# Optimization experiments

Measured on AMD Instinct MI355X. Metric: run time of the kernel, lower is better.

Reference implementation:

```python
import jax, jax.numpy as jnp
import numpy as np

NSAMPLES = [64, 32, 16, 8, 4]
TEMPERATURE = 1.0


def square_distance(src, dst):
    # src [B,N,C], dst [B,M,C] -> [B,N,M]
    d = -2.0 * jnp.einsum('bnc,bmc->bnm', src, dst)
    d = d + jnp.sum(src ** 2, -1)[:, :, None]
    d = d + jnp.sum(dst ** 2, -1)[:, None, :]
    return d


def knn_point(nsample, xyz, new_xyz):
    # indices of nsample nearest points in xyz for each query in new_xyz
    sqrdists = square_distance(new_xyz, xyz)           # [B,S,N]
    _, idx = jax.lax.top_k(-sqrdists, nsample)         # smallest distances
    return idx                                         # [B,S,nsample]


def index_points(points, idx):
    # points [B,N,C], idx [B,S,K] -> [B,S,K,C]
    B, S, K = idx.shape
    flat = idx.reshape(B, S * K)
    out = jnp.take_along_axis(points, flat[..., None], axis=1)
    return out.reshape(B, S, K, points.shape[-1])


def boundary_loss(labels, coords, feats, num_classes):
    onehot = jax.nn.one_hot(labels, num_classes, dtype=jnp.float32)  # [B,N,C]
    loss = jnp.float32(0.0)
    for i, (coord, feat) in enumerate(zip(coords, feats)):
        if i == 0:
            probability_labels = onehot
        else:
            kneighbors = i * 4
            nb_idx = knn_point(kneighbors, coords[0], coord)          # [B,Ni,k]
            probability_labels = index_points(onehot, nb_idx).mean(-2)  # [B,Ni,C]
        nsample = NSAMPLES[i]
        neighbor_indexs = knn_point(nsample, coord, coord)            # [B,Ni,ns]
        neighbor_labels = index_points(probability_labels, neighbor_indexs)  # [B,Ni,ns,C]
        neighbor_feats = index_points(feat, neighbor_indexs)          # [B,Ni,ns,D]
        center_label = jnp.argmax(probability_labels, -1)[:, :, None]  # [B,Ni,1]
        neighbor_label = jnp.argmax(neighbor_labels, -1)               # [B,Ni,ns]
        mask = (center_label == neighbor_label)                        # [B,Ni,ns] bool
        cnt = jnp.sum(mask.astype(jnp.int32), -1)
        point_mask = (cnt > 0) & (cnt < nsample)                       # [B,Ni]
        any_pm = jnp.any(point_mask)
        pm = point_mask.astype(jnp.float32)[:, :, None]                # [B,Ni,1]
        # pairwise feature distances to the nsample neighbors
        diff = feat[:, :, None, :] - neighbor_feats                    # [B,Ni,ns,D]
        dist = jnp.sqrt(jnp.sum(diff ** 2, -1) + 1e-6)                 # [B,Ni,ns]
        dist = -dist
        dist = dist - jnp.max(dist, -1, keepdims=True)
        dist = dist / TEMPERATURE
        exp = jnp.exp(dist)
        pos = jnp.sum(exp * mask.astype(jnp.float32) * pm)
        neg = jnp.sum(exp * pm)
        pos = jnp.where(any_pm, pos, 1.0)
        neg = jnp.where(any_pm, neg, 1.0)
        term = -jnp.log(pos / (neg + 1e-6))
        loss = loss + jnp.where(any_pm, term, 0.0)
    return loss


def setup_inputs() -> dict:
    key = jax.random.key(0)
    ks = jax.random.split(key, 12)
    B, N = 2, 4096
    sizes = [N, N // 4, N // 16, N // 64, N // 256]
    inp = {}
    inp['labels'] = jax.random.randint(ks[0], (B, N), 0, 21)
    for i, s in enumerate(sizes):
        inp[f'coord{i}'] = jax.random.normal(ks[1 + i], (B, s, 3), dtype=jnp.float32)
        inp[f'feat{i}'] = jax.random.normal(ks[6 + i], (B, s, 32), dtype=jnp.float32)
    inp['num_classes'] = 21
    return inp


def reference(labels, coord0, coord1, coord2, coord3, coord4,
              feat0, feat1, feat2, feat3, feat4, num_classes):
    coords = [coord0, coord1, coord2, coord3, coord4]
    feats = [feat0, feat1, feat2, feat3, feat4]
    return boundary_loss(labels, coords, feats, num_classes)
```

## Files before the change

kernel.cpp:

```cpp
#include <hip/hip_runtime.h>
#include <math.h>

#define WAVE 64
#define NC 21

__device__ __forceinline__ unsigned f32_ord(float f) {
    unsigned u = __float_as_uint(f);
    return (u & 0x80000000u) ? ~u : (u | 0x80000000u);
}

__device__ __forceinline__ int wave_sum_i32(int v) {
#pragma unroll
    for (int off = 32; off >= 1; off >>= 1)
        v += __shfl_xor(v, off, WAVE);
    return v;
}

__device__ __forceinline__ unsigned wave_min_u32(unsigned v) {
#pragma unroll
    for (int off = 32; off >= 1; off >>= 1) {
        unsigned o = (unsigned)__shfl_xor((int)v, off, WAVE);
        v = (o < v) ? o : v;
    }
    return v;
}

__device__ __forceinline__ unsigned wave_max_u32(unsigned v) {
#pragma unroll
    for (int off = 32; off >= 1; off >>= 1) {
        unsigned o = (unsigned)__shfl_xor((int)v, off, WAVE);
        v = (o > v) ? o : v;
    }
    return v;
}

__device__ __forceinline__ unsigned long long wave_min_u64(unsigned long long v) {
#pragma unroll
    for (int off = 32; off >= 1; off >>= 1) {
        unsigned long long o = __shfl_xor(v, off, WAVE);
        v = (o < v) ? o : v;
    }
    return v;
}

__device__ __forceinline__ float wave_max_f32(float v) {
#pragma unroll
    for (int off = 32; off >= 1; off >>= 1)
        v = fmaxf(v, __shfl_xor(v, off, WAVE));
    return v;
}

__device__ __forceinline__ float wave_sum_f32(float v) {
#pragma unroll
    for (int off = 32; off >= 1; off >>= 1)
        v += __shfl_xor(v, off, WAVE);
    return v;
}

__device__ __forceinline__ unsigned long long bitonic_sort64(
    unsigned long long v, int lane)
{
#pragma unroll
    for (int k = 2; k <= 64; k <<= 1) {
#pragma unroll
        for (int j = k >> 1; j > 0; j >>= 1) {
            unsigned long long o = __shfl_xor(v, j, WAVE);
            bool take_min = (((lane & j) == 0) == ((lane & k) == 0));
            unsigned long long mn = (v < o) ? v : o;
            unsigned long long mx = (v < o) ? o : v;
            v = take_min ? mn : mx;
        }
    }
    return v;
}

struct SelShm {
    unsigned long long cbuf[64];
    unsigned long long mw[4];
    int sel[64];
    int swv[4][4];
    unsigned smin[4], smax[4];
    int scnt, bcnt;
};

template <int NI, int NS>
__device__ __forceinline__ void block_topNS(
    const float4* __restrict__ pts,
    float qx, float qy, float qz, float nq,
    SelShm& shm, int tid)
{
    constexpr int NPL = (NI + 255) / 256;
    constexpr bool FULL = (NPL * 256 == NI);
    constexpr int CAP = 48;
    const int lane = tid & 63;
    const int wid = tid >> 6;
    const unsigned long long lmask = (1ull << lane) - 1ull;

    unsigned ok[NPL];
#pragma unroll
    for (int j = 0; j < NPL; ++j) {
        int g = j * 256 + tid;
        unsigned o = 0xFFFFFFFFu;
        if (FULL || g < NI) {
            float4 p = pts[g];
            float dot = qx * p.x + qy * p.y + qz * p.z;
            o = f32_ord(-2.0f * dot + nq + p.w);
        }
        ok[j] = o;
    }

    unsigned mn = 0xFFFFFFFFu, mx = 0u;
#pragma unroll
    for (int j = 0; j < NPL; ++j) {
        mn = (ok[j] < mn) ? ok[j] : mn;
        unsigned v = (ok[j] == 0xFFFFFFFFu) ? 0u : ok[j];
        mx = (v > mx) ? v : mx;
    }
    mn = wave_min_u32(mn);
    mx = wave_max_u32(mx);
    if (lane == 0) { shm.smin[wid] = mn; shm.smax[wid] = mx; }
    if (tid == 0)  { shm.scnt = 0; shm.bcnt = 0; }
    __syncthreads();
#pragma unroll
    for (int w = 0; w < 4; ++w) {
        unsigned a = shm.smin[w], b = shm.smax[w];
        mn = (a < mn) ? a : mn;
        mx = (b > mx) ? b : mx;
    }

    unsigned lo = mn, hi = mx;
    int cLo = 0, cHi = NI;
    int it = 0;
    while (lo < hi && (cHi - cLo) > CAP) {
        unsigned piv = lo + ((hi - lo) >> 1);
        int c = 0;
#pragma unroll
        for (int j = 0; j < NPL; ++j) c += (ok[j] <= piv) ? 1 : 0;
        c = wave_sum_i32(c);
        if (lane == 0) shm.swv[it & 3][wid] = c;
        __syncthreads();
        int tot = shm.swv[it & 3][0] + shm.swv[it & 3][1]
                + shm.swv[it & 3][2] + shm.swv[it & 3][3];
        if (tot >= NS) { hi = piv; cHi = tot; }
        else           { lo = piv + 1; cLo = tot; }
        ++it;
    }

    const int clt = cLo;
    const int R = NS - cLo;

#pragma unroll
    for (int j = 0; j < NPL; ++j) {
        bool s = ok[j] < lo;
        unsigned long long mk = __ballot(s);
        int n = __popcll(mk);
        if (n) {
            int wb = 0;
            if (lane == 0) wb = atomicAdd(&shm.scnt, n);
            wb = __shfl(wb, 0, WAVE);
            if (s) shm.sel[wb + __popcll(mk & lmask)] = j * 256 + tid;
        }
    }
#pragma unroll
    for (int j = 0; j < NPL; ++j) {
        bool s = (ok[j] >= lo) && (ok[j] <= hi);
        unsigned long long mk = __ballot(s);
        int n = __popcll(mk);
        if (n) {
            int wb = 0;
            if (lane == 0) wb = atomicAdd(&shm.bcnt, n);
            wb = __shfl(wb, 0, WAVE);
            int slot = wb + __popcll(mk & lmask);
            if (s && slot < 64)
                shm.cbuf[slot] =
                    ((unsigned long long)ok[j] << 32) | (unsigned)(j * 256 + tid);
        }
    }
    __syncthreads();
    int Bcnt = shm.bcnt;

    if (Bcnt <= 64) {
        if (wid == 0) {
            unsigned long long p = (lane < Bcnt) ? shm.cbuf[lane] : ~0ull;
            p = bitonic_sort64(p, lane);
            if (lane < R) shm.sel[clt + lane] = (int)(unsigned)p;
        }
        __syncthreads();
    } else {
        unsigned consumed = 0u;
        for (int r = 0; r < R; ++r) {
            unsigned long long mv = ~0ull;
#pragma unroll
            for (int j = 0; j < NPL; ++j) {
                bool s = (ok[j] >= lo) && (ok[j] <= hi) && !((consumed >> j) & 1u);
                unsigned long long p =
                    ((unsigned long long)ok[j] << 32) | (unsigned)(j * 256 + tid);
                mv = (s && p < mv) ? p : mv;
            }
            mv = wave_min_u64(mv);
            if (lane == 0) shm.mw[wid] = mv;
            __syncthreads();
            unsigned long long m0 = shm.mw[0], m1 = shm.mw[1];
            unsigned long long m2 = shm.mw[2], m3 = shm.mw[3];
            unsigned long long ta = (m0 < m1) ? m0 : m1;
            unsigned long long tb = (m2 < m3) ? m2 : m3;
            unsigned long long t = (ta < tb) ? ta : tb;
#pragma unroll
            for (int j = 0; j < NPL; ++j) {
                unsigned long long p =
                    ((unsigned long long)ok[j] << 32) | (unsigned)(j * 256 + tid);
                if (p == t) consumed |= 1u << j;
            }
            if (tid == 0) shm.sel[clt + r] = (int)(unsigned)t;
            __syncthreads();
        }
    }
}

template <int NQ, int K>
__device__ __forceinline__ void knn_level(
    const float* __restrict__ qc, const float4* __restrict__ pk0,
    const int* __restrict__ rl, int* __restrict__ out,
    int q, SelShm& shm, int tid)
{
    int b = q / NQ, qi = q - b * NQ;
    const float* qp = qc + ((long)b * NQ + qi) * 3;
    float qx = qp[0], qy = qp[1], qz = qp[2];
    float nq = qx * qx + qy * qy + qz * qz;
    block_topNS<4096, K>(pk0 + (long)b * 4096, qx, qy, qz, nq, shm, tid);
    if ((tid >> 6) == 0) {
        int lane = tid & 63;
        int lb = (lane < K) ? rl[(long)b * 4096 + shm.sel[lane]] : -1;
        int cnt = 0;
#pragma unroll
        for (int k = 0; k < K; ++k) {
            int lk = __shfl(lb, k, WAVE);
            cnt += (lk == lane) ? 1 : 0;
        }
        int key = (lane < NC) ? ((cnt << 8) | (255 - lane)) : 0;
#pragma unroll
        for (int off = 32; off >= 1; off >>= 1) {
            int o = __shfl_xor(key, off, WAVE);
            key = (o > key) ? o : key;
        }
        if (lane == 0) out[(long)b * NQ + qi] = 255 - (key & 255);
    }
}

template <int NI, int NS>
__device__ __forceinline__ void boundary_epilogue(
    const float* __restrict__ feat, const int* __restrict__ lbl,
    double* __restrict__ pos, double* __restrict__ neg, int* __restrict__ anyf,
    int b, int qi, int lane, int nb)
{
    int center = lbl[(long)b * NI + qi];
    bool m = false;
    float dj = -INFINITY;
    if (lane < NS) {
        m = (lbl[(long)b * NI + nb] == center);
        const float4* fq = (const float4*)(feat + ((long)b * NI + qi) * 32);
        const float4* fn = (const float4*)(feat + ((long)b * NI + nb) * 32);
        float s = 0.f;
#pragma unroll
        for (int d = 0; d < 8; ++d) {
            float4 a = fq[d], c = fn[d];
            float d0 = a.x - c.x, d1 = a.y - c.y;
            float d2 = a.z - c.z, d3 = a.w - c.w;
            s += d0 * d0 + d1 * d1 + d2 * d2 + d3 * d3;
        }
        dj = -sqrtf(s + 1e-6f);
    }
    unsigned long long mb = __ballot(m);
    int cnt = __popcll(mb);
    float mxv = wave_max_f32(dj);
    float ej = 0.f, pj = 0.f;
    if (lane < NS) {
        ej = expf(dj - mxv);
        pj = m ? ej : 0.f;
    }
    float se = wave_sum_f32(ej);
    float sp = wave_sum_f32(pj);
    bool pm = (cnt > 0) && (cnt < NS);
    if (pm && lane == 0) {
        atomicAdd(pos, (double)sp);
        atomicAdd(neg, (double)se);
        *anyf = 1;
    }
}

template <int NI, int NS>
__device__ __forceinline__ void boundary_level(
    const float4* __restrict__ pk, const float* __restrict__ coord,
    const float* __restrict__ feat, const int* __restrict__ lbl,
    double* __restrict__ pos, double* __restrict__ neg, int* __restrict__ anyf,
    int q, SelShm& shm, int tid)
{
    int b = q / NI, qi = q - b * NI;
    const float* qp = coord + ((long)b * NI + qi) * 3;
    float qx = qp[0], qy = qp[1], qz = qp[2];
    float nq = qx * qx + qy * qy + qz * qz;
    block_topNS<NI, NS>(pk + (long)b * NI, qx, qy, qz, nq, shm, tid);
    if ((tid >> 6) == 0)
        boundary_epilogue<NI, NS>(feat, lbl, pos, neg, anyf,
                                  b, qi, tid & 63, shm.sel[tid & 63]);
}

template <int NI, int NS>
__device__ __forceinline__ void small_boundary_level(
    const float4* __restrict__ pk, const float* __restrict__ coord,
    const float* __restrict__ feat, const int* __restrict__ lbl,
    double* __restrict__ pos, double* __restrict__ neg, int* __restrict__ anyf,
    int q, int tid)
{
    if (tid >= 64) return;
    int lane = tid;
    int b = q / NI, qi = q - b * NI;
    const float* qp = coord + ((long)b * NI + qi) * 3;
    float qx = qp[0], qy = qp[1], qz = qp[2];
    float nq = qx * qx + qy * qy + qz * qz;
    unsigned long long p = ~0ull;
    if (lane < NI) {
        float4 P = pk[(long)b * NI + lane];
        float dot = qx * P.x + qy * P.y + qz * P.z;
        unsigned o = f32_ord(-2.0f * dot + nq + P.w);
        p = ((unsigned long long)o << 32) | (unsigned)lane;
    }
    unsigned long long h = bitonic_sort64(p, lane);
    boundary_epilogue<NI, NS>(feat, lbl, pos, neg, anyf,
                              b, qi, lane, (int)(unsigned)h);
}

__global__ __launch_bounds__(256) void pack_kernel(
    const float* __restrict__ c0, const float* __restrict__ c1,
    const float* __restrict__ c2, const float* __restrict__ c3,
    const float* __restrict__ c4,
    float4* __restrict__ p0, float4* __restrict__ p1,
    float4* __restrict__ p2, float4* __restrict__ p3,
    float4* __restrict__ p4,
    double* __restrict__ posA, double* __restrict__ negA,
    int* __restrict__ anyA, int B)
{
    int idx = blockIdx.x * 256 + threadIdx.x;
    if (idx < 5) { posA[idx] = 0.0; negA[idx] = 0.0; anyA[idx] = 0; }
    int s0 = B * 4096, s1 = s0 + B * 1024, s2 = s1 + B * 256;
    int s3 = s2 + B * 64, s4 = s3 + B * 16;
    const float* src; float4* dst; int i;
    if (idx < s0)      { src = c0; dst = p0; i = idx; }
    else if (idx < s1) { src = c1; dst = p1; i = idx - s0; }
    else if (idx < s2) { src = c2; dst = p2; i = idx - s1; }
    else if (idx < s3) { src = c3; dst = p3; i = idx - s2; }
    else if (idx < s4) { src = c4; dst = p4; i = idx - s3; }
    else return;
    float x = src[3 * i], y = src[3 * i + 1], z = src[3 * i + 2];
    dst[i] = make_float4(x, y, z, x * x + y * y + z * z);
}

__global__ __launch_bounds__(256) void knn_fused(
    const float* __restrict__ c1, const float* __restrict__ c2,
    const float* __restrict__ c3, const float* __restrict__ c4,
    const float4* __restrict__ pk0, const int* __restrict__ labels,
    int* __restrict__ lbl1, int* __restrict__ lbl2,
    int* __restrict__ lbl3, int* __restrict__ lbl4, int B)
{
    __shared__ SelShm shm;
    int q = blockIdx.x, tid = threadIdx.x;
    int n1 = B * 1024, n2 = n1 + B * 256, n3 = n2 + B * 64, n4 = n3 + B * 16;
    if (q < n1)      knn_level<1024, 4>(c1, pk0, labels, lbl1, q,      shm, tid);
    else if (q < n2) knn_level<256,  8>(c2, pk0, labels, lbl2, q - n1, shm, tid);
    else if (q < n3) knn_level<64,  12>(c3, pk0, labels, lbl3, q - n2, shm, tid);
    else if (q < n4) knn_level<16,  16>(c4, pk0, labels, lbl4, q - n3, shm, tid);
}

__global__ __launch_bounds__(256) void boundary_fused(
    const float4* __restrict__ p0, const float4* __restrict__ p1,
    const float4* __restrict__ p2, const float4* __restrict__ p3,
    const float4* __restrict__ p4,
    const float* __restrict__ c0, const float* __restrict__ c1,
    const float* __restrict__ c2, const float* __restrict__ c3,
    const float* __restrict__ c4,
    const float* __restrict__ f0, const float* __restrict__ f1,
    const float* __restrict__ f2, const float* __restrict__ f3,
    const float* __restrict__ f4,
    const int* __restrict__ labels, const int* __restrict__ lbl1,
    const int* __restrict__ lbl2, const int* __restrict__ lbl3,
    const int* __restrict__ lbl4,
    double* __restrict__ posA, double* __restrict__ negA,
    int* __restrict__ anyA, int B)
{
    __shared__ SelShm shm;
    int q = blockIdx.x, tid = threadIdx.x;
    int m0 = B * 4096, m1 = m0 + B * 1024, m2 = m1 + B * 256;
    int m3 = m2 + B * 64, m4 = m3 + B * 16;
    if (q < m0)
        boundary_level<4096, 64>(p0, c0, f0, labels, posA+0, negA+0, anyA+0, q,      shm, tid);
    else if (q < m1)
        boundary_level<1024, 32>(p1, c1, f1, lbl1,   posA+1, negA+1, anyA+1, q - m0, shm, tid);
    else if (q < m2)
        boundary_level<256,  16>(p2, c2, f2, lbl2,   posA+2, negA+2, anyA+2, q - m1, shm, tid);
    else if (q < m3)
        small_boundary_level<64, 8>(p3, c3, f3, lbl3, posA+3, negA+3, anyA+3, q - m2, tid);
    else if (q < m4)
        small_boundary_level<16, 4>(p4, c4, f4, lbl4, posA+4, negA+4, anyA+4, q - m3, tid);
}

__global__ void finalize_kernel(const double* __restrict__ pos,
                                const double* __restrict__ neg,
                                const int* __restrict__ anyf,
                                float* __restrict__ out) {
    if (threadIdx.x == 0 && blockIdx.x == 0) {
        float loss = 0.f;
        for (int i = 0; i < 5; ++i) {
            if (anyf[i]) {
                float p = (float)pos[i];
                float n = (float)neg[i];
                loss += -logf(p / (n + 1e-6f));
            }
        }
        out[0] = loss;
    }
}

extern "C" void kernel_launch(void* const* d_in, const int* in_sizes, int n_in,
                              void* d_out, int out_size, void* d_ws, size_t ws_size,
                              hipStream_t stream) {
    (void)out_size; (void)ws_size;
    const int* labels = (const int*)d_in[0];
    const float* coord[5];
    const float* feat[5];
    bool interleaved = (n_in >= 3 && in_sizes[2] == 2 * 4096 * 32);
    if (interleaved) {
        for (int i = 0; i < 5; ++i) {
            coord[i] = (const float*)d_in[1 + 2 * i];
            feat[i]  = (const float*)d_in[2 + 2 * i];
        }
    } else {
        for (int i = 0; i < 5; ++i) {
            coord[i] = (const float*)d_in[1 + i];
            feat[i]  = (const float*)d_in[6 + i];
        }
    }
    int B = in_sizes[0] / 4096;

    char* ws = (char*)d_ws;
    double* posA = (double*)ws;
    double* negA = posA + 5;
    int* anyA = (int*)(negA + 5);
    int* lbl1 = anyA + 8;
    int* lbl2 = lbl1 + B * 1024;
    int* lbl3 = lbl2 + B * 256;
    int* lbl4 = lbl3 + B * 64;
    size_t off = 112 + (size_t)B * (1024 + 256 + 64 + 16) * 4;
    off = (off + 15) & ~(size_t)15;
    float4* pk0 = (float4*)(ws + off); off += (size_t)B * 4096 * 16;
    float4* pk1 = (float4*)(ws + off); off += (size_t)B * 1024 * 16;
    float4* pk2 = (float4*)(ws + off); off += (size_t)B * 256 * 16;
    float4* pk3 = (float4*)(ws + off); off += (size_t)B * 64 * 16;
    float4* pk4 = (float4*)(ws + off);

    int tot = B * (4096 + 1024 + 256 + 64 + 16);
    hipLaunchKernelGGL(pack_kernel, dim3((tot + 255) / 256), dim3(256), 0, stream,
                       coord[0], coord[1], coord[2], coord[3], coord[4],
                       pk0, pk1, pk2, pk3, pk4, posA, negA, anyA, B);

    int n4 = B * (1024 + 256 + 64 + 16);
    hipLaunchKernelGGL(knn_fused, dim3(n4), dim3(256), 0, stream,
                       coord[1], coord[2], coord[3], coord[4],
                       pk0, labels, lbl1, lbl2, lbl3, lbl4, B);

    hipLaunchKernelGGL(boundary_fused, dim3(tot), dim3(256), 0, stream,
                       pk0, pk1, pk2, pk3, pk4,
                       coord[0], coord[1], coord[2], coord[3], coord[4],
                       feat[0], feat[1], feat[2], feat[3], feat[4],
                       labels, lbl1, lbl2, lbl3, lbl4,
                       posA, negA, anyA, B);

    hipLaunchKernelGGL(finalize_kernel, dim3(1), dim3(1), 0, stream,
                       posA, negA, anyA, (float*)d_out);
}
```

Before: 401.3 us.

## Switch KNN top-k to wave-per-query selection with LDS-staged point clouds

```diff
diff --git a/kernel.cpp b/kernel.cpp
--- a/kernel.cpp
+++ b/kernel.cpp
@@ -13,24 +13,6 @@
 #pragma unroll
     for (int off = 32; off >= 1; off >>= 1)
         v += __shfl_xor(v, off, WAVE);
-    return v;
-}
-
-__device__ __forceinline__ unsigned wave_min_u32(unsigned v) {
-#pragma unroll
-    for (int off = 32; off >= 1; off >>= 1) {
-        unsigned o = (unsigned)__shfl_xor((int)v, off, WAVE);
-        v = (o < v) ? o : v;
-    }
-    return v;
-}
-
-__device__ __forceinline__ unsigned wave_max_u32(unsigned v) {
-#pragma unroll
-    for (int off = 32; off >= 1; off >>= 1) {
-        unsigned o = (unsigned)__shfl_xor((int)v, off, WAVE);
-        v = (o > v) ? o : v;
-    }
     return v;
 }
 
@@ -74,177 +56,145 @@
     return v;
 }
 
-struct SelShm {
-    unsigned long long cbuf[64];
-    unsigned long long mw[4];
-    int sel[64];
-    int swv[4][4];
-    unsigned smin[4], smax[4];
-    int scnt, bcnt;
-};
+__device__ __forceinline__ unsigned long long bitonic_merge_keep_low(
+    unsigned long long h, unsigned long long c, int lane)
+{
+    unsigned long long cr = __shfl(c, 63 - lane, WAVE);
+    unsigned long long v = (h < cr) ? h : cr;
+#pragma unroll
+    for (int j = 32; j > 0; j >>= 1) {
+        unsigned long long o = __shfl_xor(v, j, WAVE);
+        bool take_min = ((lane & j) == 0);
+        unsigned long long mn = (v < o) ? v : o;
+        unsigned long long mx = (v < o) ? o : v;
+        v = take_min ? mn : mx;
+    }
+    return v;
+}
+
+__device__ __forceinline__ unsigned long long cand_u64(
+    const float4* __restrict__ spts, int ch, int lane,
+    float qx, float qy, float qz, float nq)
+{
+    int g = ch * 64 + lane;
+    float4 p = spts[g];
+    float dot = qx * p.x + qy * p.y + qz * p.z;
+    unsigned o = f32_ord(-2.0f * dot + nq + p.w);
+    return ((unsigned long long)o << 32) | (unsigned)g;
+}
 
 template <int NI, int NS>
-__device__ __forceinline__ void block_topNS(
-    const float4* __restrict__ pts,
+__device__ __forceinline__ void wave_select(
+    const float4* __restrict__ spts,
     float qx, float qy, float qz, float nq,
-    SelShm& shm, int tid)
-{
-    constexpr int NPL = (NI + 255) / 256;
-    constexpr bool FULL = (NPL * 256 == NI);
-    constexpr int CAP = 48;
-    const int lane = tid & 63;
-    const int wid = tid >> 6;
-    const unsigned long long lmask = (1ull << lane) - 1ull;
-
-    unsigned ok[NPL];
-#pragma unroll
-    for (int j = 0; j < NPL; ++j) {
-        int g = j * 256 + tid;
-        unsigned o = 0xFFFFFFFFu;
-        if (FULL || g < NI) {
-            float4 p = pts[g];
-            float dot = qx * p.x + qy * p.y + qz * p.z;
-            o = f32_ord(-2.0f * dot + nq + p.w);
-        }
-        ok[j] = o;
-    }
-
-    unsigned mn = 0xFFFFFFFFu, mx = 0u;
-#pragma unroll
-    for (int j = 0; j < NPL; ++j) {
-        mn = (ok[j] < mn) ? ok[j] : mn;
-        unsigned v = (ok[j] == 0xFFFFFFFFu) ? 0u : ok[j];
-        mx = (v > mx) ? v : mx;
-    }
-    mn = wave_min_u32(mn);
-    mx = wave_max_u32(mx);
-    if (lane == 0) { shm.smin[wid] = mn; shm.smax[wid] = mx; }
-    if (tid == 0)  { shm.scnt = 0; shm.bcnt = 0; }
-    __syncthreads();
-#pragma unroll
-    for (int w = 0; w < 4; ++w) {
-        unsigned a = shm.smin[w], b = shm.smax[w];
-        mn = (a < mn) ? a : mn;
-        mx = (b > mx) ? b : mx;
-    }
-
-    unsigned lo = mn, hi = mx;
-    int cLo = 0, cHi = NI;
-    int it = 0;
-    while (lo < hi && (cHi - cLo) > CAP) {
-        unsigned piv = lo + ((hi - lo) >> 1);
-        int c = 0;
-#pragma unroll
-        for (int j = 0; j < NPL; ++j) c += (ok[j] <= piv) ? 1 : 0;
-        c = wave_sum_i32(c);
-        if (lane == 0) shm.swv[it & 3][wid] = c;
-        __syncthreads();
-        int tot = shm.swv[it & 3][0] + shm.swv[it & 3][1]
-                + shm.swv[it & 3][2] + shm.swv[it & 3][3];
-        if (tot >= NS) { hi = piv; cHi = tot; }
-        else           { lo = piv + 1; cLo = tot; }
-        ++it;
-    }
-
-    const int clt = cLo;
-    const int R = NS - cLo;
-
-#pragma unroll
-    for (int j = 0; j < NPL; ++j) {
-        bool s = ok[j] < lo;
-        unsigned long long mk = __ballot(s);
-        int n = __popcll(mk);
-        if (n) {
-            int wb = 0;
-            if (lane == 0) wb = atomicAdd(&shm.scnt, n);
-            wb = __shfl(wb, 0, WAVE);
-            if (s) shm.sel[wb + __popcll(mk & lmask)] = j * 256 + tid;
-        }
-    }
-#pragma unroll
-    for (int j = 0; j < NPL; ++j) {
-        bool s = (ok[j] >= lo) && (ok[j] <= hi);
-        unsigned long long mk = __ballot(s);
-        int n = __popcll(mk);
-        if (n) {
-            int wb = 0;
-            if (lane == 0) wb = atomicAdd(&shm.bcnt, n);
-            wb = __shfl(wb, 0, WAVE);
-            int slot = wb + __popcll(mk & lmask);
-            if (s && slot < 64)
-                shm.cbuf[slot] =
-                    ((unsigned long long)ok[j] << 32) | (unsigned)(j * 256 + tid);
-        }
-    }
-    __syncthreads();
-    int Bcnt = shm.bcnt;
-
-    if (Bcnt <= 64) {
-        if (wid == 0) {
-            unsigned long long p = (lane < Bcnt) ? shm.cbuf[lane] : ~0ull;
-            p = bitonic_sort64(p, lane);
-            if (lane < R) shm.sel[clt + lane] = (int)(unsigned)p;
-        }
-        __syncthreads();
+    int* __restrict__ sel,
+    unsigned long long* __restrict__ band,
+    int lane)
+{
+    constexpr int NCH = NI / 64;
+    const unsigned long long lm = (1ull << lane) - 1ull;
+
+    unsigned long long mnu = ~0ull;
+#pragma unroll 4
+    for (int ch = 0; ch < NCH; ++ch) {
+        unsigned long long u = cand_u64(spts, ch, lane, qx, qy, qz, nq);
+        mnu = (u < mnu) ? u : mnu;
+    }
+    unsigned long long S = bitonic_sort64(mnu, lane);
+
+    constexpr int D = (NS >= 8) ? (NS / 8) : 1;
+    unsigned long long tj[6];
+    int pj[6];
+#pragma unroll
+    for (int j = 0; j < 6; ++j) {
+        pj[j] = NS - 1 - j * D;
+        tj[j] = __shfl(S, (pj[j] >= 0) ? pj[j] : 0, WAVE);
+    }
+
+    unsigned long long msk[6] = {0ull, 0ull, 0ull, 0ull, 0ull, 0ull};
+#pragma unroll 4
+    for (int ch = 0; ch < NCH; ++ch) {
+        unsigned long long u = cand_u64(spts, ch, lane, qx, qy, qz, nq);
+        unsigned long long bit = 1ull << ch;
+#pragma unroll
+        for (int j = 0; j < 6; ++j)
+            msk[j] |= (u <= tj[j]) ? bit : 0ull;
+    }
+    int c[6];
+#pragma unroll
+    for (int j = 0; j < 6; ++j) {
+        c[j] = wave_sum_i32(__popcll(msk[j]));
+        if (pj[j] < 0) c[j] = -1;
+    }
+    int js = 0;
+#pragma unroll
+    for (int j = 1; j < 6; ++j) if (c[j] >= NS) js = j;
+
+    int Cb = 0;
+    unsigned long long mA = 0ull;
+    if (js < 5 && pj[js + 1] >= 0) { Cb = c[js + 1]; mA = msk[js + 1]; }
+
+    unsigned long long bmask = msk[js] & ~mA;
+    int bandM = c[js] - Cb;
+    int R = NS - Cb;
+
+    if (Cb > 0) {
+        int base = 0;
+#pragma unroll 4
+        for (int ch = 0; ch < NCH; ++ch) {
+            bool a = (mA >> ch) & 1ull;
+            unsigned long long mk = __ballot(a);
+            if (a) sel[base + __popcll(mk & lm)] = ch * 64 + lane;
+            base += __popcll(mk);
+        }
+    }
+
+    if (bandM == R) {
+        int base = Cb;
+#pragma unroll 4
+        for (int ch = 0; ch < NCH; ++ch) {
+            bool s = (bmask >> ch) & 1ull;
+            unsigned long long mk = __ballot(s);
+            if (s) sel[base + __popcll(mk & lm)] = ch * 64 + lane;
+            base += __popcll(mk);
+        }
+    } else if (bandM <= 128) {
+        int base = 0;
+#pragma unroll 4
+        for (int ch = 0; ch < NCH; ++ch) {
+            bool s = (bmask >> ch) & 1ull;
+            unsigned long long mk = __ballot(s);
+            if (s) band[base + __popcll(mk & lm)] =
+                       cand_u64(spts, ch, lane, qx, qy, qz, nq);
+            base += __popcll(mk);
+        }
+        __threadfence_block();
+        unsigned long long v0 = (lane < bandM) ? band[lane] : ~0ull;
+        v0 = bitonic_sort64(v0, lane);
+        if (bandM > 64) {
+            unsigned long long v1 = (64 + lane < bandM) ? band[64 + lane] : ~0ull;
+            v1 = bitonic_sort64(v1, lane);
+            v0 = bitonic_merge_keep_low(v0, v1, lane);
+        }
+        if (lane < R) sel[Cb + lane] = (int)(unsigned)v0;
     } else {
-        unsigned consumed = 0u;
-        for (int r = 0; r < R; ++r) {
-            unsigned long long mv = ~0ull;
-#pragma unroll
-            for (int j = 0; j < NPL; ++j) {
-                bool s = (ok[j] >= lo) && (ok[j] <= hi) && !((consumed >> j) & 1u);
-                unsigned long long p =
-                    ((unsigned long long)ok[j] << 32) | (unsigned)(j * 256 + tid);
-                mv = (s && p < mv) ? p : mv;
+        unsigned long long cons = 0ull;
+        for (int r = 0; r < NS; ++r) {
+            unsigned long long best = ~0ull;
+#pragma unroll 4
+            for (int ch = 0; ch < NCH; ++ch) {
+                if (!((cons >> ch) & 1ull)) {
+                    unsigned long long u = cand_u64(spts, ch, lane, qx, qy, qz, nq);
+                    best = (u < best) ? u : best;
+                }
             }
-            mv = wave_min_u64(mv);
-            if (lane == 0) shm.mw[wid] = mv;
-            __syncthreads();
-            unsigned long long m0 = shm.mw[0], m1 = shm.mw[1];
-            unsigned long long m2 = shm.mw[2], m3 = shm.mw[3];
-            unsigned long long ta = (m0 < m1) ? m0 : m1;
-            unsigned long long tb = (m2 < m3) ? m2 : m3;
-            unsigned long long t = (ta < tb) ? ta : tb;
-#pragma unroll
-            for (int j = 0; j < NPL; ++j) {
-                unsigned long long p =
-                    ((unsigned long long)ok[j] << 32) | (unsigned)(j * 256 + tid);
-                if (p == t) consumed |= 1u << j;
-            }
-            if (tid == 0) shm.sel[clt + r] = (int)(unsigned)t;
-            __syncthreads();
-        }
-    }
-}
-
-template <int NQ, int K>
-__device__ __forceinline__ void knn_level(
-    const float* __restrict__ qc, const float4* __restrict__ pk0,
-    const int* __restrict__ rl, int* __restrict__ out,
-    int q, SelShm& shm, int tid)
-{
-    int b = q / NQ, qi = q - b * NQ;
-    const float* qp = qc + ((long)b * NQ + qi) * 3;
-    float qx = qp[0], qy = qp[1], qz = qp[2];
-    float nq = qx * qx + qy * qy + qz * qz;
-    block_topNS<4096, K>(pk0 + (long)b * 4096, qx, qy, qz, nq, shm, tid);
-    if ((tid >> 6) == 0) {
-        int lane = tid & 63;
-        int lb = (lane < K) ? rl[(long)b * 4096 + shm.sel[lane]] : -1;
-        int cnt = 0;
-#pragma unroll
-        for (int k = 0; k < K; ++k) {
-            int lk = __shfl(lb, k, WAVE);
-            cnt += (lk == lane) ? 1 : 0;
-        }
-        int key = (lane < NC) ? ((cnt << 8) | (255 - lane)) : 0;
-#pragma unroll
-        for (int off = 32; off >= 1; off >>= 1) {
-            int o = __shfl_xor(key, off, WAVE);
-            key = (o > key) ? o : key;
-        }
-        if (lane == 0) out[(long)b * NQ + qi] = 255 - (key & 255);
-    }
+            best = wave_min_u64(best);
+            unsigned gi = (unsigned)best;
+            if ((gi & 63u) == (unsigned)lane) cons |= 1ull << (gi >> 6);
+            if (lane == 0) sel[r] = (int)gi;
+        }
+    }
+    __threadfence_block();
 }
 
 template <int NI, int NS>
@@ -288,87 +238,83 @@
     }
 }
 
+template <int K>
+__device__ __forceinline__ void knn_epilogue(
+    const int* __restrict__ rl, int* __restrict__ out,
+    long b, int out_idx, int lane, const int* __restrict__ sel)
+{
+    int lb = (lane < K) ? rl[b * 4096 + sel[lane]] : -1;
+    int cnt = 0;
+#pragma unroll
+    for (int k = 0; k < K; ++k) {
+        int lk = __shfl(lb, k, WAVE);
+        cnt += (lk == lane) ? 1 : 0;
+    }
+    int key = (lane < NC) ? ((cnt << 8) | (255 - lane)) : 0;
+#pragma unroll
+    for (int off = 32; off >= 1; off >>= 1) {
+        int o = __shfl_xor(key, off, WAVE);
+        key = (o > key) ? o : key;
+    }
+    if (lane == 0) out[out_idx] = 255 - (key & 255);
+}
+
+struct Shm {
+    float4 pts[4096];
+    int sel[4][64];
+    unsigned long long band[4][128];
+};
+
 template <int NI, int NS>
-__device__ __forceinline__ void boundary_level(
-    const float4* __restrict__ pk, const float* __restrict__ coord,
+__device__ __forceinline__ void bnd_sec(
+    int sblk, const float4* __restrict__ pk, const float* __restrict__ qc,
     const float* __restrict__ feat, const int* __restrict__ lbl,
-    double* __restrict__ pos, double* __restrict__ neg, int* __restrict__ anyf,
-    int q, SelShm& shm, int tid)
-{
-    int b = q / NI, qi = q - b * NI;
-    const float* qp = coord + ((long)b * NI + qi) * 3;
-    float qx = qp[0], qy = qp[1], qz = qp[2];
-    float nq = qx * qx + qy * qy + qz * qz;
-    block_topNS<NI, NS>(pk + (long)b * NI, qx, qy, qz, nq, shm, tid);
-    if ((tid >> 6) == 0)
-        boundary_epilogue<NI, NS>(feat, lbl, pos, neg, anyf,
-                                  b, qi, tid & 63, shm.sel[tid & 63]);
+    double* pos, double* neg, int* anyf, Shm& shm, int tid)
+{
+    int b = (sblk * 16) / NI;
+    for (int i = tid; i < NI; i += 256) shm.pts[i] = pk[(long)b * NI + i];
+    __syncthreads();
+    int w = tid >> 6, lane = tid & 63;
+    int q0 = sblk * 16 + w * 4;
+#pragma unroll 1
+    for (int i = 0; i < 4; ++i) {
+        int q = q0 + i;
+        int qi = q - b * NI;
+        const float* qp = qc + ((long)b * NI + qi) * 3;
+        float qx = qp[0], qy = qp[1], qz = qp[2];
+        float nq = qx * qx + qy * qy + qz * qz;
+        wave_select<NI, NS>(shm.pts, qx, qy, qz, nq,
+                            shm.sel[w], shm.band[w], lane);
+        boundary_epilogue<NI, NS>(feat, lbl, pos, neg, anyf, b, qi, lane,
+                                  (lane < NS) ? shm.sel[w][lane] : 0);
+    }
 }
 
 template <int NI, int NS>
-__device__ __forceinline__ void small_boundary_level(
-    const float4* __restrict__ pk, const float* __restrict__ coord,
+__device__ __forceinline__ void small_sec(
+    int sblk, const float4* __restrict__ pk, const float* __restrict__ qc,
     const float* __restrict__ feat, const int* __restrict__ lbl,
-    double* __restrict__ pos, double* __restrict__ neg, int* __restrict__ anyf,
-    int q, int tid)
-{
-    if (tid >= 64) return;
-    int lane = tid;
-    int b = q / NI, qi = q - b * NI;
-    const float* qp = coord + ((long)b * NI + qi) * 3;
-    float qx = qp[0], qy = qp[1], qz = qp[2];
-    float nq = qx * qx + qy * qy + qz * qz;
-    unsigned long long p = ~0ull;
-    if (lane < NI) {
-        float4 P = pk[(long)b * NI + lane];
-        float dot = qx * P.x + qy * P.y + qz * P.z;
-        unsigned o = f32_ord(-2.0f * dot + nq + P.w);
-        p = ((unsigned long long)o << 32) | (unsigned)lane;
-    }
-    unsigned long long h = bitonic_sort64(p, lane);
-    boundary_epilogue<NI, NS>(feat, lbl, pos, neg, anyf,
-                              b, qi, lane, (int)(unsigned)h);
-}
-
-__global__ __launch_bounds__(256) void pack_kernel(
-    const float* __restrict__ c0, const float* __restrict__ c1,
-    const float* __restrict__ c2, const float* __restrict__ c3,
-    const float* __restrict__ c4,
-    float4* __restrict__ p0, float4* __restrict__ p1,
-    float4* __restrict__ p2, float4* __restrict__ p3,
-    float4* __restrict__ p4,
-    double* __restrict__ posA, double* __restrict__ negA,
-    int* __restrict__ anyA, int B)
-{
-    int idx = blockIdx.x * 256 + threadIdx.x;
-    if (idx < 5) { posA[idx] = 0.0; negA[idx] = 0.0; anyA[idx] = 0; }
-    int s0 = B * 4096, s1 = s0 + B * 1024, s2 = s1 + B * 256;
-    int s3 = s2 + B * 64, s4 = s3 + B * 16;
-    const float* src; float4* dst; int i;
-    if (idx < s0)      { src = c0; dst = p0; i = idx; }
-    else if (idx < s1) { src = c1; dst = p1; i = idx - s0; }
-    else if (idx < s2) { src = c2; dst = p2; i = idx - s1; }
-    else if (idx < s3) { src = c3; dst = p3; i = idx - s2; }
-    else if (idx < s4) { src = c4; dst = p4; i = idx - s3; }
-    else return;
-    float x = src[3 * i], y = src[3 * i + 1], z = src[3 * i + 2];
-    dst[i] = make_float4(x, y, z, x * x + y * y + z * z);
-}
-
-__global__ __launch_bounds__(256) void knn_fused(
-    const float* __restrict__ c1, const float* __restrict__ c2,
-    const float* __restrict__ c3, const float* __restrict__ c4,
-    const float4* __restrict__ pk0, const int* __restrict__ labels,
-    int* __restrict__ lbl1, int* __restrict__ lbl2,
-    int* __restrict__ lbl3, int* __restrict__ lbl4, int B)
-{
-    __shared__ SelShm shm;
-    int q = blockIdx.x, tid = threadIdx.x;
-    int n1 = B * 1024, n2 = n1 + B * 256, n3 = n2 + B * 64, n4 = n3 + B * 16;
-    if (q < n1)      knn_level<1024, 4>(c1, pk0, labels, lbl1, q,      shm, tid);
-    else if (q < n2) knn_level<256,  8>(c2, pk0, labels, lbl2, q - n1, shm, tid);
-    else if (q < n3) knn_level<64,  12>(c3, pk0, labels, lbl3, q - n2, shm, tid);
-    else if (q < n4) knn_level<16,  16>(c4, pk0, labels, lbl4, q - n3, shm, tid);
+    double* pos, double* neg, int* anyf, int tid)
+{
+    int w = tid >> 6, lane = tid & 63;
+#pragma unroll 1
+    for (int i = 0; i < 4; ++i) {
+        int q = sblk * 16 + w * 4 + i;
+        int b = q / NI, qi = q - b * NI;
+        const float* qp = qc + ((long)b * NI + qi) * 3;
+        float qx = qp[0], qy = qp[1], qz = qp[2];
+        float nq = qx * qx + qy * qy + qz * qz;
+        unsigned long long p = ~0ull;
+        if (lane < NI) {
+            float4 P = pk[(long)b * NI + lane];
+            float dot = qx * P.x + qy * P.y + qz * P.z;
+            unsigned o = f32_ord(-2.0f * dot + nq + P.w);
+            p = ((unsigned long long)o << 32) | (unsigned)lane;
+        }
+        unsigned long long h = bitonic_sort64(p, lane);
+        boundary_epilogue<NI, NS>(feat, lbl, pos, neg, anyf, b, qi, lane,
+                                  (int)(unsigned)h);
+    }
 }
 
 __global__ __launch_bounds__(256) void boundary_fused(
@@ -387,20 +333,85 @@
     double* __restrict__ posA, double* __restrict__ negA,
     int* __restrict__ anyA, int B)
 {
-    __shared__ SelShm shm;
-    int q = blockIdx.x, tid = threadIdx.x;
-    int m0 = B * 4096, m1 = m0 + B * 1024, m2 = m1 + B * 256;
-    int m3 = m2 + B * 64, m4 = m3 + B * 16;
-    if (q < m0)
-        boundary_level<4096, 64>(p0, c0, f0, labels, posA+0, negA+0, anyA+0, q,      shm, tid);
-    else if (q < m1)
-        boundary_level<1024, 32>(p1, c1, f1, lbl1,   posA+1, negA+1, anyA+1, q - m0, shm, tid);
-    else if (q < m2)
-        boundary_level<256,  16>(p2, c2, f2, lbl2,   posA+2, negA+2, anyA+2, q - m1, shm, tid);
-    else if (q < m3)
-        small_boundary_level<64, 8>(p3, c3, f3, lbl3, posA+3, negA+3, anyA+3, q - m2, tid);
-    else if (q < m4)
-        small_boundary_level<16, 4>(p4, c4, f4, lbl4, posA+4, negA+4, anyA+4, q - m3, tid);
+    __shared__ Shm shm;
+    int blk = blockIdx.x, tid = threadIdx.x;
+    int s0 = B * 4096 / 16, s1 = s0 + B * 1024 / 16, s2 = s1 + B * 256 / 16;
+    int s3 = s2 + B * 64 / 16, s4 = s3 + B * 16 / 16;
+    if (blk < s0)
+        bnd_sec<4096, 64>(blk, p0, c0, f0, labels, posA+0, negA+0, anyA+0, shm, tid);
+    else if (blk < s1)
+        bnd_sec<1024, 32>(blk - s0, p1, c1, f1, lbl1, posA+1, negA+1, anyA+1, shm, tid);
+    else if (blk < s2)
+        bnd_sec<256, 16>(blk - s1, p2, c2, f2, lbl2, posA+2, negA+2, anyA+2, shm, tid);
+    else if (blk < s3)
+        small_sec<64, 8>(blk - s2, p3, c3, f3, lbl3, posA+3, negA+3, anyA+3, tid);
+    else if (blk < s4)
+        small_sec<16, 4>(blk - s3, p4, c4, f4, lbl4, posA+4, negA+4, anyA+4, tid);
+}
+
+template <int NQ, int K>
+__device__ __forceinline__ void knn_sec(
+    int sblk, const float4* __restrict__ pk0, const float* __restrict__ qc,
+    const int* __restrict__ rl, int* __restrict__ out, Shm& shm, int tid)
+{
+    int b = (sblk * 16) / NQ;
+    for (int i = tid; i < 4096; i += 256) shm.pts[i] = pk0[(long)b * 4096 + i];
+    __syncthreads();
+    int w = tid >> 6, lane = tid & 63;
+    int q0 = sblk * 16 + w * 4;
+#pragma unroll 1
+    for (int i = 0; i < 4; ++i) {
+        int q = q0 + i;
+        int qi = q - b * NQ;
+        const float* qp = qc + ((long)b * NQ + qi) * 3;
+        float qx = qp[0], qy = qp[1], qz = qp[2];
+        float nq = qx * qx + qy * qy + qz * qz;
+        wave_select<4096, K>(shm.pts, qx, qy, qz, nq,
+                             shm.sel[w], shm.band[w], lane);
+        knn_epilogue<K>(rl, out, b, (int)((long)b * NQ + qi), lane, shm.sel[w]);
+    }
+}
+
+__global__ __launch_bounds__(256) void knn_fused(
+    const float* __restrict__ c1, const float* __restrict__ c2,
+    const float* __restrict__ c3, const float* __restrict__ c4,
+    const float4* __restrict__ pk0, const int* __restrict__ labels,
+    int* __restrict__ lbl1, int* __restrict__ lbl2,
+    int* __restrict__ lbl3, int* __restrict__ lbl4, int B)
+{
+    __shared__ Shm shm;
+    int blk = blockIdx.x, tid = threadIdx.x;
+    int n1 = B * 1024 / 16, n2 = n1 + B * 256 / 16;
+    int n3 = n2 + B * 64 / 16, n4 = n3 + B * 16 / 16;
+    if (blk < n1)      knn_sec<1024, 4>(blk,      pk0, c1, labels, lbl1, shm, tid);
+    else if (blk < n2) knn_sec<256,  8>(blk - n1, pk0, c2, labels, lbl2, shm, tid);
+    else if (blk < n3) knn_sec<64,  12>(blk - n2, pk0, c3, labels, lbl3, shm, tid);
+    else if (blk < n4) knn_sec<16,  16>(blk - n3, pk0, c4, labels, lbl4, shm, tid);
+}
+
+__global__ __launch_bounds__(256) void pack_kernel(
+    const float* __restrict__ c0, const float* __restrict__ c1,
+    const float* __restrict__ c2, const float* __restrict__ c3,
+    const float* __restrict__ c4,
+    float4* __restrict__ p0, float4* __restrict__ p1,
+    float4* __restrict__ p2, float4* __restrict__ p3,
+    float4* __restrict__ p4,
+    double* __restrict__ posA, double* __restrict__ negA,
+    int* __restrict__ anyA, int B)
+{
+    int idx = blockIdx.x * 256 + threadIdx.x;
+    if (idx < 5) { posA[idx] = 0.0; negA[idx] = 0.0; anyA[idx] = 0; }
+    int s0 = B * 4096, s1 = s0 + B * 1024, s2 = s1 + B * 256;
+    int s3 = s2 + B * 64, s4 = s3 + B * 16;
+    const float* src; float4* dst; int i;
+    if (idx < s0)      { src = c0; dst = p0; i = idx; }
+    else if (idx < s1) { src = c1; dst = p1; i = idx - s0; }
+    else if (idx < s2) { src = c2; dst = p2; i = idx - s1; }
+    else if (idx < s3) { src = c3; dst = p3; i = idx - s2; }
+    else if (idx < s4) { src = c4; dst = p4; i = idx - s3; }
+    else return;
+    float x = src[3 * i], y = src[3 * i + 1], z = src[3 * i + 2];
+    dst[i] = make_float4(x, y, z, x * x + y * y + z * z);
 }
 
 __global__ void finalize_kernel(const double* __restrict__ pos,
@@ -462,12 +473,13 @@
                        coord[0], coord[1], coord[2], coord[3], coord[4],
                        pk0, pk1, pk2, pk3, pk4, posA, negA, anyA, B);
 
-    int n4 = B * (1024 + 256 + 64 + 16);
-    hipLaunchKernelGGL(knn_fused, dim3(n4), dim3(256), 0, stream,
+    int knn_blocks = B * (1024 + 256 + 64 + 16) / 16;
+    hipLaunchKernelGGL(knn_fused, dim3(knn_blocks), dim3(256), 0, stream,
                        coord[1], coord[2], coord[3], coord[4],
                        pk0, labels, lbl1, lbl2, lbl3, lbl4, B);
 
-    hipLaunchKernelGGL(boundary_fused, dim3(tot), dim3(256), 0, stream,
+    int bnd_blocks = B * (4096 + 1024 + 256 + 64 + 16) / 16;
+    hipLaunchKernelGGL(boundary_fused, dim3(bnd_blocks), dim3(256), 0, stream,
                        pk0, pk1, pk2, pk3, pk4,
                        coord[0], coord[1], coord[2], coord[3], coord[4],
                        feat[0], feat[1], feat[2], feat[3], feat[4],
```

Result: slower. 464.8 us (+15.8%).
